# Optimization experiments

Measured on AMD Instinct MI355X. Metric: run time of the kernel, lower is better.

Reference implementation:

```python
import jax, jax.numpy as jnp
import numpy as np

B, D = 90000, 100
E_GNN, E_MLP = 4, 4
E = E_GNN + E_MLP + 1  # 9
K = 2
NOISE_EPS = 0.01
LOSS_COEF = 0.4
GATE_MEAN, GATE_STD = 0.1, 1.0  # registered buffers in the torch module


def setup_inputs() -> dict:
    key = jax.random.key(0)
    ks = jax.random.split(key, 16)
    f = jax.random.normal
    return {
        "memory_feats": f(ks[0], (B, D), jnp.float32),
        "recent_raw": f(ks[1], (B, E_MLP, D), jnp.float32),
        "spatial_raw": f(ks[2], (B, E_GNN, D), jnp.float32),
        "node_feats_src": f(ks[3], (B, D), jnp.float32),
        "noise": f(ks[4], (B, E), jnp.float32),
        "deg_coef": f(ks[5], (1, D, 2), jnp.float32),
        "w_gate": f(ks[6], (6 * D, E), jnp.float32) * 0.05,
        "w_noise": f(ks[7], (6 * D, E), jnp.float32) * 0.05,
        "src_w": f(ks[8], (D, D), jnp.float32) * 0.1,
        "src_b": f(ks[9], (D,), jnp.float32) * 0.1,
        "dst_w": f(ks[10], (D, D), jnp.float32) * 0.1,
        "dst_b": f(ks[11], (D,), jnp.float32) * 0.1,
        "out_w": f(ks[12], (D, 1), jnp.float32) * 0.1,
        "out_b": f(ks[13], (1,), jnp.float32) * 0.1,
        "degree": jax.random.randint(ks[14], (B,), 0, 64, jnp.int32),
        "neg_samples": 1,
    }


def _cv_squared(x):
    # torch .var() is unbiased (ddof=1)
    return jnp.var(x, ddof=1) / (jnp.mean(x) ** 2 + 1e-10)


def _norm_cdf(v):
    return jax.scipy.stats.norm.cdf(v, loc=GATE_MEAN, scale=GATE_STD)


def reference(memory_feats, recent_raw, spatial_raw, node_feats_src, noise,
              deg_coef, w_gate, w_noise, src_w, src_b, dst_w, dst_b,
              out_w, out_b, degree, neg_samples):
    # memory expert output (dropout is identity in eval; relu applied)
    mem = jax.nn.relu(memory_feats)                        # [B, D]
    rec = jax.nn.relu(recent_raw)                          # [B, Em, D]
    log_deg = jnp.log(degree.astype(mem.dtype) + 1.0)      # [B]
    # degree-conditioned reweighting: stack([r, r*log_deg],-1) * deg_coef, sum(-1)
    c0, c1 = deg_coef[0, :, 0], deg_coef[0, :, 1]          # [D]
    spa = spatial_raw * (c0 + log_deg[:, None, None] * c1)  # [B, Eg, D]

    combine = jnp.concatenate([mem[:, None, :], spa, rec], axis=1)  # [B, E, D]
    result_spa = spa.mean(axis=1)
    result_rec = rec.mean(axis=1)
    x1 = mem + result_spa + result_rec
    x2 = mem * result_spa * result_rec
    cat = jnp.concatenate([mem, result_spa, result_rec, x1, x2, node_feats_src], axis=1)  # [B, 6D]

    # noisy top-k gating (train=True)
    clean = cat @ w_gate                                   # [B, E]
    std = jax.nn.softplus(cat @ w_noise) + NOISE_EPS
    noisy = clean + noise * std
    top_vals, top_idx = jax.lax.top_k(noisy, K + 1)        # [B, K+1]
    topk_gates = jax.nn.softmax(top_vals[:, :K], axis=1)
    b_idx = jnp.arange(noisy.shape[0])[:, None]
    gates = jnp.zeros_like(noisy).at[b_idx, top_idx[:, :K]].set(topk_gates)

    # prob of being in top-k for load-balance loss
    thr_in = top_vals[:, K][:, None]
    thr_out = top_vals[:, K - 1][:, None]
    is_in = noisy > thr_in
    prob = jnp.where(is_in,
                     _norm_cdf((clean - thr_in) / std),
                     _norm_cdf((clean - thr_out) / std))
    load = prob.sum(axis=0)
    importance = gates.sum(axis=0)
    loss = LOSS_COEF * (_cv_squared(importance) + _cv_squared(load))

    out = jnp.einsum('bed,be->bd', combine, gates)         # [B, D]

    # edge predictor
    num_edge = out.shape[0] // (neg_samples + 2)
    h_src = out[:num_edge] @ src_w + src_b
    h_pos = out[num_edge:2 * num_edge] @ dst_w + dst_b
    h_neg = out[2 * num_edge:] @ dst_w + dst_b
    pos = jax.nn.relu(h_src + h_pos) @ out_w + out_b       # [num_edge, 1]
    neg = jax.nn.relu(jnp.tile(h_src, (neg_samples, 1)) + h_neg) @ out_w + out_b
    return pos, neg, loss
```

## Files before the change

kernel.cpp:

```cpp
#include <hip/hip_runtime.h>
#include <math.h>

#define DD 100

#define DPP_ADD(v, ctrl) ((v) + __int_as_float(__builtin_amdgcn_update_dpp( \
    0, __float_as_int(v), (ctrl), 0xf, 0xf, true)))

__device__ __forceinline__ float blo(unsigned u){
  union { unsigned i; float f; } c; c.i = u << 16; return c.f;
}
__device__ __forceinline__ float bhi(unsigned u){
  union { unsigned i; float f; } c; c.i = u & 0xFFFF0000u; return c.f;
}
__device__ __forceinline__ unsigned short f2bf(float f){
  unsigned u = __float_as_uint(f);
  unsigned r = (u + 0x7FFFu + ((u >> 16) & 1u)) >> 16;
  return (unsigned short)r;
}
__device__ __forceinline__ float phi_fast(float z){
  float x  = z * 0.70710678118654752440f;
  float ax = fabsf(x);
  float t  = __builtin_amdgcn_rcpf(1.0f + 0.3275911f*ax);
  float p  = t*(0.254829592f + t*(-0.284496736f + t*(1.421413741f
           + t*(-1.453152027f + t*1.061405429f))));
  float e  = __expf(-ax*ax);
  float erfv = copysignf(1.0f - p*e, x);
  return 0.5f*(1.0f + erfv);
}
__device__ __forceinline__ float4 relu4(float4 v){
  return make_float4(fmaxf(v.x,0.f), fmaxf(v.y,0.f), fmaxf(v.z,0.f), fmaxf(v.w,0.f));
}

__global__ __launch_bounds__(256) void k_gate(
    const float* __restrict__ memf, const float* __restrict__ recr,
    const float* __restrict__ spar, const float* __restrict__ nsrc,
    const float* __restrict__ noise, const float* __restrict__ degc,
    const float* __restrict__ wg,   const float* __restrict__ wn,
    const int*   __restrict__ degree,
    float4* __restrict__ gateinfo, float* __restrict__ partials, int B)
{
  __shared__ __align__(16) float sWF[100*92];
  __shared__ __align__(16) float sC0[DD], sC1[DD];
  __shared__ float sPart[4][18];

  for (int i = threadIdx.x; i < 9000; i += 256){
    int d = i / 90, j2 = i % 90;
    int seg = j2 / 18, e = j2 % 18;
    int rowA = (seg==0) ? d : (seg==1) ? 100+d : (seg==2) ? 200+d
             : (seg==3) ? 400+d : 500+d;
    const float* W = (e < 9) ? wg : wn;
    int ee = (e < 9) ? e : e - 9;
    float v = W[rowA*9 + ee] + ((seg < 3) ? W[(300+d)*9 + ee] : 0.f);
    sWF[d*92 + j2] = v;
  }
  for (int i = threadIdx.x; i < DD; i += 256){ sC0[i]=degc[2*i]; sC1[i]=degc[2*i+1]; }
  __syncthreads();

  const int wave = threadIdx.x >> 6, lane = threadIdx.x & 63;
  const int fq = lane & 3, rl = lane >> 2;
  const float4* sC04 = (const float4*)sC0;
  const float4* sC14 = (const float4*)sC1;

  float ldA[9], imA[9];
  #pragma unroll
  for (int e = 0; e < 9; e++){ ldA[e]=0.f; imA[e]=0.f; }

  const int row = (blockIdx.x*4 + wave)*16 + rl;
  const bool valid = row < B;
  const int rc = valid ? row : B-1;
  {
    const float* pm = memf + (size_t)rc*DD;
    const float* ps = spar + (size_t)rc*4*DD;
    const float* pr = recr + (size_t)rc*4*DD;
    const float* pn = nsrc + (size_t)rc*DD;
    float ldg = __logf((float)degree[rc] + 1.0f);

    float cg[9], cn[9];
    #pragma unroll
    for (int e = 0; e < 9; e++){ cg[e]=0.f; cn[e]=0.f; }

    for (int k = 0; k < 7; k++){
      int c = fq + 4*k;
      float fz = (c < 25) ? 1.f : 0.f;
      int ce = (c < 25) ? c : 0;
      float4 me = *(const float4*)(pm + 4*ce);
      float4 s0 = *(const float4*)(ps + 0*DD + 4*ce);
      float4 s1 = *(const float4*)(ps + 1*DD + 4*ce);
      float4 s2 = *(const float4*)(ps + 2*DD + 4*ce);
      float4 s3 = *(const float4*)(ps + 3*DD + 4*ce);
      float4 r0 = *(const float4*)(pr + 0*DD + 4*ce);
      float4 r1 = *(const float4*)(pr + 1*DD + 4*ce);
      float4 r2 = *(const float4*)(pr + 2*DD + 4*ce);
      float4 r3 = *(const float4*)(pr + 3*DD + 4*ce);
      float4 nv = *(const float4*)(pn + 4*ce);
      float4 c04 = sC04[ce], c14 = sC14[ce];

      float4 m4 = relu4(me);
      float4 sc = make_float4(c04.x + ldg*c14.x, c04.y + ldg*c14.y,
                              c04.z + ldg*c14.z, c04.w + ldg*c14.w);
      float4 rs4 = make_float4((s0.x+s1.x+s2.x+s3.x)*0.25f*sc.x,
                               (s0.y+s1.y+s2.y+s3.y)*0.25f*sc.y,
                               (s0.z+s1.z+s2.z+s3.z)*0.25f*sc.z,
                               (s0.w+s1.w+s2.w+s3.w)*0.25f*sc.w);
      float4 a0 = relu4(r0), a1 = relu4(r1), a2 = relu4(r2), a3 = relu4(r3);
      float4 rr4 = make_float4((a0.x+a1.x+a2.x+a3.x)*0.25f,
                               (a0.y+a1.y+a2.y+a3.y)*0.25f,
                               (a0.z+a1.z+a2.z+a3.z)*0.25f,
                               (a0.w+a1.w+a2.w+a3.w)*0.25f);
      m4.x*=fz; m4.y*=fz; m4.z*=fz; m4.w*=fz;
      rs4.x*=fz; rs4.y*=fz; rs4.z*=fz; rs4.w*=fz;
      rr4.x*=fz; rr4.y*=fz; rr4.z*=fz; rr4.w*=fz;
      float4 ns4 = make_float4(nv.x*fz, nv.y*fz, nv.z*fz, nv.w*fz);
      float4 x24 = make_float4(m4.x*rs4.x*rr4.x, m4.y*rs4.y*rr4.y,
                               m4.z*rs4.z*rr4.z, m4.w*rs4.w*rr4.w);

      #pragma unroll
      for (int j = 0; j < 4; j++){
        const float der0 = (j==0)?m4.x :(j==1)?m4.y :(j==2)?m4.z :m4.w;
        const float der1 = (j==0)?rs4.x:(j==1)?rs4.y:(j==2)?rs4.z:rs4.w;
        const float der2 = (j==0)?rr4.x:(j==1)?rr4.y:(j==2)?rr4.z:rr4.w;
        const float der3 = (j==0)?x24.x:(j==1)?x24.y:(j==2)?x24.z:x24.w;
        const float der4 = (j==0)?ns4.x:(j==1)?ns4.y:(j==2)?ns4.z:ns4.w;
        const float4* wpj = (const float4*)(sWF + (4*ce + j)*92);
        #pragma unroll
        for (int t = 0; t < 23; t++){
          float4 w = wpj[t];
          #pragma unroll
          for (int u = 0; u < 4; u++){
            const int ww = 4*t + u;
            if (ww < 90){
              const int seg = ww/18, e = ww%18;
              float wv = (u==0)?w.x:(u==1)?w.y:(u==2)?w.z:w.w;
              float dv = (seg==0)?der0:(seg==1)?der1:(seg==2)?der2:(seg==3)?der3:der4;
              if (e < 9) cg[e] += dv*wv; else cn[e-9] += dv*wv;
            }
          }
        }
      }
    }

    #pragma unroll
    for (int e = 0; e < 9; e++){
      cg[e] = DPP_ADD(cg[e], 0xB1); cg[e] = DPP_ADD(cg[e], 0x4E);
      cn[e] = DPP_ADD(cn[e], 0xB1); cn[e] = DPP_ADD(cn[e], 0x4E);
    }

    float sd[9], rsd[9], nz[9];
    #pragma unroll
    for (int e = 0; e < 9; e++){
      float x = cn[e];
      float spl = fmaxf(x, 0.f) + __logf(1.0f + __expf(-fabsf(x)));
      sd[e]  = spl + 0.01f;
      rsd[e] = __builtin_amdgcn_rcpf(sd[e]);
      nz[e]  = cg[e] + noise[(size_t)rc*9 + e] * sd[e];
    }
    float v1 = -3.402823e38f, v2 = v1, v3 = v1; int i1 = -1, i2 = -1;
    #pragma unroll
    for (int e = 0; e < 9; e++){
      float v = nz[e];
      if (v > v1){ v3=v2; v2=v1; i2=i1; v1=v; i1=e; }
      else if (v > v2){ v3=v2; v2=v; i2=e; }
      else if (v > v3){ v3=v; }
    }
    float t  = __expf(v2 - v1);
    float g1 = __builtin_amdgcn_rcpf(1.0f + t);
    float g2 = t*g1;
    if (valid){
      #pragma unroll
      for (int e = 0; e < 9; e++){
        float thr = (nz[e] > v3) ? v3 : v2;
        float z = (cg[e] - thr)*rsd[e] - 0.1f;
        ldA[e] += phi_fast(z);
        imA[e] += (e==i1) ? g1 : ((e==i2) ? g2 : 0.f);
      }
      if (fq == 0)
        gateinfo[row] = make_float4(g1, g2, __int_as_float(i1), __int_as_float(i2));
    }
  }

  #pragma unroll
  for (int e = 0; e < 9; e++){
    #pragma unroll
    for (int off = 4; off < 64; off <<= 1){
      ldA[e] += __shfl_xor(ldA[e], off, 64);
      imA[e] += __shfl_xor(imA[e], off, 64);
    }
  }
  if (lane == 0){
    #pragma unroll
    for (int e = 0; e < 9; e++){ sPart[wave][e] = imA[e]; sPart[wave][9+e] = ldA[e]; }
  }
  __syncthreads();
  if (threadIdx.x < 18){
    float s = sPart[0][threadIdx.x] + sPart[1][threadIdx.x]
            + sPart[2][threadIdx.x] + sPart[3][threadIdx.x];
    partials[blockIdx.x*18 + threadIdx.x] = s;
  }
}

__global__ __launch_bounds__(256) void k_mix(
    const float* __restrict__ memf, const float* __restrict__ recr,
    const float* __restrict__ spar, const float* __restrict__ degc,
    const int* __restrict__ degree, const float4* __restrict__ gateinfo,
    float* __restrict__ outm, int B)
{
  const int total = B*25;
  for (int idx = blockIdx.x*256 + threadIdx.x; idx < total; idx += gridDim.x*256){
    int row = idx / 25, q = idx - row*25;
    float4 gi = gateinfo[row];
    float gv[2] = {gi.x, gi.y};
    int   ei[2] = {__float_as_int(gi.z), __float_as_int(gi.w)};
    float4 acc = make_float4(0.f,0.f,0.f,0.f);
    #pragma unroll
    for (int s = 0; s < 2; s++){
      int e = ei[s]; float g = gv[s];
      float4 v;
      if (e == 0){
        v = relu4(*(const float4*)(memf + (size_t)row*DD + 4*q));
      } else if (e < 5){
        float ldg = __logf((float)degree[row] + 1.0f);
        float4 ca = *(const float4*)(degc + 8*q);
        float4 cb = *(const float4*)(degc + 8*q + 4);
        float4 sv = *(const float4*)(spar + ((size_t)row*4 + (e-1))*DD + 4*q);
        v = make_float4(sv.x*(ca.x + ldg*ca.y), sv.y*(ca.z + ldg*ca.w),
                        sv.z*(cb.x + ldg*cb.y), sv.w*(cb.z + ldg*cb.w));
      } else {
        v = relu4(*(const float4*)(recr + ((size_t)row*4 + (e-5))*DD + 4*q));
      }
      acc.x += g*v.x; acc.y += g*v.y; acc.z += g*v.z; acc.w += g*v.w;
    }
    ((float4*)outm)[(size_t)row*25 + q] = acc;
  }
}

__global__ __launch_bounds__(1024) void k_loss(const float* __restrict__ partials,
                                               int nblk, float* __restrict__ dloss)
{
  __shared__ float sS[18][57];
  int t = threadIdx.x;
  if (t < 1008){
    int k = t % 18, c = t / 18;
    float s = 0.f;
    for (int b = c; b < nblk; b += 56) s += partials[b*18 + k];
    sS[k][c] = s;
  }
  __syncthreads();
  if (t < 18){
    float tot = 0.f;
    #pragma unroll
    for (int c = 0; c < 56; c++) tot += sS[t][c];
    sS[t][56] = tot;
  }
  __syncthreads();
  if (t == 0){
    float mi = 0.f, ml = 0.f;
    #pragma unroll
    for (int e = 0; e < 9; e++){ mi += sS[e][56]; ml += sS[9+e][56]; }
    mi *= (1.f/9.f); ml *= (1.f/9.f);
    float vi = 0.f, vl = 0.f;
    #pragma unroll
    for (int e = 0; e < 9; e++){
      float a = sS[e][56]   - mi; vi += a*a;
      float b = sS[9+e][56] - ml; vl += b*b;
    }
    vi *= (1.f/8.f); vl *= (1.f/8.f);
    *dloss = 0.4f * (vi/(mi*mi + 1e-10f) + vl/(ml*ml + 1e-10f));
  }
}

__global__ __launch_bounds__(512) void k_edge(
    const float* __restrict__ om,
    const float* __restrict__ sw, const float* __restrict__ sb,
    const float* __restrict__ dw, const float* __restrict__ db,
    const float* __restrict__ ow, const float* __restrict__ ob,
    float* __restrict__ dout, int NE)
{
  __shared__ __align__(4) unsigned short sSW[DD*102];
  __shared__ __align__(4) unsigned short sDW[DD*102];
  __shared__ float sSB[DD], sDB[DD], sOW[DD];

  for (int i = threadIdx.x; i < DD*DD; i += 512){
    int k = i / DD, d = i % DD;
    sSW[d*102 + k] = f2bf(sw[i]);
    sDW[d*102 + k] = f2bf(dw[i]);
  }
  for (int i = threadIdx.x; i < DD; i += 512){ sSB[i]=sb[i]; sDB[i]=db[i]; sOW[i]=ow[i]; }
  __syncthreads();

  const int wave = threadIdx.x >> 6, lane = threadIdx.x & 63;
  const int grp = blockIdx.x*8 + wave;
  const int e0 = grp*4;
  if (e0 >= NE) return;
  const int e0u = __builtin_amdgcn_readfirstlane(e0);
  const float* oS = om + (size_t)e0u*DD;
  const float* oP = om + ((size_t)(NE  + e0u))*DD;
  const float* oN = om + ((size_t)(2*NE + e0u))*DD;
  const int d0 = lane, d1 = lane + 64;
  const bool h1 = (d1 < DD);
  const int dc1 = h1 ? d1 : 0;

  float aS[4][2], aP[4][2], aN[4][2];
  #pragma unroll
  for (int r = 0; r < 4; r++){
    aS[r][0]=0.f; aS[r][1]=0.f; aP[r][0]=0.f; aP[r][1]=0.f; aN[r][0]=0.f; aN[r][1]=0.f;
  }

  for (int k = 0; k < DD; k += 4){
    unsigned uA = *(const unsigned*)&sSW[d0 *102 + k];
    unsigned uB = *(const unsigned*)&sSW[d0 *102 + k + 2];
    unsigned uC = *(const unsigned*)&sSW[dc1*102 + k];
    unsigned uD = *(const unsigned*)&sSW[dc1*102 + k + 2];
    unsigned uE = *(const unsigned*)&sDW[d0 *102 + k];
    unsigned uF = *(const unsigned*)&sDW[d0 *102 + k + 2];
    unsigned uG = *(const unsigned*)&sDW[dc1*102 + k];
    unsigned uH = *(const unsigned*)&sDW[dc1*102 + k + 2];
    float wS00=blo(uA), wS01=bhi(uA), wS02=blo(uB), wS03=bhi(uB);
    float wS10=blo(uC), wS11=bhi(uC), wS12=blo(uD), wS13=bhi(uD);
    float wD00=blo(uE), wD01=bhi(uE), wD02=blo(uF), wD03=bhi(uF);
    float wD10=blo(uG), wD11=bhi(uG), wD12=blo(uH), wD13=bhi(uH);
    #pragma unroll
    for (int r = 0; r < 4; r++){
      float4 ov = *(const float4*)(oS + r*DD + k);
      float4 pv = *(const float4*)(oP + r*DD + k);
      float4 nv = *(const float4*)(oN + r*DD + k);
      aS[r][0] += ov.x*wS00 + ov.y*wS01 + ov.z*wS02 + ov.w*wS03;
      aS[r][1] += ov.x*wS10 + ov.y*wS11 + ov.z*wS12 + ov.w*wS13;
      aP[r][0] += pv.x*wD00 + pv.y*wD01 + pv.z*wD02 + pv.w*wD03;
      aP[r][1] += pv.x*wD10 + pv.y*wD11 + pv.z*wD12 + pv.w*wD13;
      aN[r][0] += nv.x*wD00 + nv.y*wD01 + nv.z*wD02 + nv.w*wD03;
      aN[r][1] += nv.x*wD10 + nv.y*wD11 + nv.z*wD12 + nv.w*wD13;
    }
  }

  float owa = sOW[d0], owb = sOW[dc1];
  float sba = sSB[d0], sbb = sSB[dc1];
  float dba = sDB[d0], dbb = sDB[dc1];
  float ob0 = ob[0];
  #pragma unroll
  for (int r = 0; r < 4; r++){
    float hs0 = aS[r][0] + sba, hp0 = aP[r][0] + dba, hn0 = aN[r][0] + dba;
    float tp = fmaxf(hs0 + hp0, 0.f)*owa;
    float tn = fmaxf(hs0 + hn0, 0.f)*owa;
    if (h1){
      float hs1 = aS[r][1] + sbb, hp1 = aP[r][1] + dbb, hn1 = aN[r][1] + dbb;
      tp += fmaxf(hs1 + hp1, 0.f)*owb;
      tn += fmaxf(hs1 + hn1, 0.f)*owb;
    }
    #pragma unroll
    for (int off = 32; off > 0; off >>= 1){
      tp += __shfl_xor(tp, off, 64);
      tn += __shfl_xor(tn, off, 64);
    }
    if (lane == 0){
      dout[e0 + r]      = tp + ob0;
      dout[NE + e0 + r] = tn + ob0;
    }
  }
}

extern "C" void kernel_launch(void* const* d_in, const int* in_sizes, int n_in,
                              void* d_out, int out_size, void* d_ws, size_t ws_size,
                              hipStream_t stream)
{
  (void)n_in; (void)out_size; (void)ws_size;
  const float* memf  = (const float*)d_in[0];
  const float* recr  = (const float*)d_in[1];
  const float* spar  = (const float*)d_in[2];
  const float* nsrc  = (const float*)d_in[3];
  const float* noise = (const float*)d_in[4];
  const float* degc  = (const float*)d_in[5];
  const float* wg    = (const float*)d_in[6];
  const float* wn    = (const float*)d_in[7];
  const float* sw    = (const float*)d_in[8];
  const float* sb    = (const float*)d_in[9];
  const float* dw    = (const float*)d_in[10];
  const float* db    = (const float*)d_in[11];
  const float* ow    = (const float*)d_in[12];
  const float* ob    = (const float*)d_in[13];
  const int*   deg   = (const int*)d_in[14];

  const int B  = in_sizes[0] / DD;
  const int NE = B / 3;
  const int blocksA = (B + 63) / 64;

  float4* gateinfo = (float4*)d_ws;
  float*  outm     = (float*)(gateinfo + B);
  float*  partials = outm + (size_t)B*DD;
  float*  dout     = (float*)d_out;

  k_gate<<<dim3(blocksA), dim3(256), 0, stream>>>(memf, recr, spar, nsrc, noise,
                                                  degc, wg, wn, deg, gateinfo,
                                                  partials, B);
  k_mix<<<dim3(2048), dim3(256), 0, stream>>>(memf, recr, spar, degc, deg,
                                              gateinfo, outm, B);
  k_loss<<<dim3(1), dim3(1024), 0, stream>>>(partials, blocksA, dout + 2*NE);
  const int blocks2 = (NE/4 + 7) / 8;
  k_edge<<<dim3(blocks2), dim3(512), 0, stream>>>(outm, sw, sb, dw, db, ow, ob, dout, NE);
}
```

Measured before the change: 286.1 us.

## Move gate weight folding to separate kernel and give each row its own thread

The folded gate/noise weight matrix is now built once by a small k_fold kernel into workspace, replacing the per-block rebuild into shared memory. k_gate shrinks to 64-thread blocks with one thread per row. Each thread walks all 25 float4 chunks with double-buffered register loads, and reads the weights through uniform global/scalar loads, which removes the DPP cross-lane reduction and the block sync. The trade-offs are a per-thread stride of 1600 bytes across rows, which gives uncoalesced input loads, higher register pressure, and an extra kernel launch.

```diff
diff --git a/kernel.cpp b/kernel.cpp
--- a/kernel.cpp
+++ b/kernel.cpp
@@ -2,9 +2,6 @@
 #include <math.h>
 
 #define DD 100
-
-#define DPP_ADD(v, ctrl) ((v) + __int_as_float(__builtin_amdgcn_update_dpp( \
-    0, __float_as_int(v), (ctrl), 0xf, 0xf, true)))
 
 __device__ __forceinline__ float blo(unsigned u){
   union { unsigned i; float f; } c; c.i = u << 16; return c.f;
@@ -31,170 +28,139 @@
   return make_float4(fmaxf(v.x,0.f), fmaxf(v.y,0.f), fmaxf(v.z,0.f), fmaxf(v.w,0.f));
 }
 
-__global__ __launch_bounds__(256) void k_gate(
+__global__ void k_fold(const float* __restrict__ wg, const float* __restrict__ wn,
+                       float* __restrict__ wfold)
+{
+  int idx = blockIdx.x*256 + threadIdx.x;
+  if (idx >= 9000) return;
+  int dim = idx/90, r = idx%90, s = r/18, e = r%18;
+  const float* W = (e < 9) ? wg : wn;
+  int ee = (e < 9) ? e : e-9;
+  int rowA = (s==0) ? dim : (s==1) ? 100+dim : (s==2) ? 200+dim
+           : (s==3) ? 400+dim : 500+dim;
+  float v = W[rowA*9 + ee] + ((s < 3) ? W[(300+dim)*9 + ee] : 0.f);
+  wfold[idx] = v;
+}
+
+struct Quad { float4 me, s0, s1, s2, s3, r0, r1, r2, r3, nv; };
+
+__device__ __forceinline__ void loadq(Quad& Q, const float* pm, const float* ps,
+                                      const float* pr, const float* pn, int q){
+  Q.me = *(const float4*)(pm + 4*q);
+  Q.s0 = *(const float4*)(ps + 0*DD + 4*q);
+  Q.s1 = *(const float4*)(ps + 1*DD + 4*q);
+  Q.s2 = *(const float4*)(ps + 2*DD + 4*q);
+  Q.s3 = *(const float4*)(ps + 3*DD + 4*q);
+  Q.r0 = *(const float4*)(pr + 0*DD + 4*q);
+  Q.r1 = *(const float4*)(pr + 1*DD + 4*q);
+  Q.r2 = *(const float4*)(pr + 2*DD + 4*q);
+  Q.r3 = *(const float4*)(pr + 3*DD + 4*q);
+  Q.nv = *(const float4*)(pn + 4*q);
+}
+
+#define GETJ(v) ((j==0)?(v).x:(j==1)?(v).y:(j==2)?(v).z:(v).w)
+
+__device__ __forceinline__ void bodyq(const Quad& Q, const float* __restrict__ wfold,
+                                      const float* __restrict__ degc, float ldg,
+                                      float* cg, float* cn, int q){
+  #pragma unroll
+  for (int j = 0; j < 4; j++){
+    const int dim = 4*q + j;
+    float c0 = degc[2*dim], c1 = degc[2*dim+1];
+    float mm = fmaxf(GETJ(Q.me), 0.f);
+    float sc = c0 + ldg*c1;
+    float rs = (GETJ(Q.s0)+GETJ(Q.s1)+GETJ(Q.s2)+GETJ(Q.s3))*0.25f*sc;
+    float rr = (fmaxf(GETJ(Q.r0),0.f)+fmaxf(GETJ(Q.r1),0.f)
+               +fmaxf(GETJ(Q.r2),0.f)+fmaxf(GETJ(Q.r3),0.f))*0.25f;
+    float x2 = mm*rs*rr;
+    float ns = GETJ(Q.nv);
+    const float* w = wfold + (size_t)dim*90;
+    #pragma unroll
+    for (int e = 0; e < 9; e++){
+      cg[e] += mm*w[e]    + rs*w[18+e] + rr*w[36+e] + x2*w[54+e] + ns*w[72+e];
+      cn[e] += mm*w[9+e]  + rs*w[27+e] + rr*w[45+e] + x2*w[63+e] + ns*w[81+e];
+    }
+  }
+}
+
+__global__ __launch_bounds__(64) void k_gate(
     const float* __restrict__ memf, const float* __restrict__ recr,
     const float* __restrict__ spar, const float* __restrict__ nsrc,
     const float* __restrict__ noise, const float* __restrict__ degc,
-    const float* __restrict__ wg,   const float* __restrict__ wn,
-    const int*   __restrict__ degree,
+    const float* __restrict__ wfold, const int* __restrict__ degree,
     float4* __restrict__ gateinfo, float* __restrict__ partials, int B)
 {
-  __shared__ __align__(16) float sWF[100*92];
-  __shared__ __align__(16) float sC0[DD], sC1[DD];
-  __shared__ float sPart[4][18];
-
-  for (int i = threadIdx.x; i < 9000; i += 256){
-    int d = i / 90, j2 = i % 90;
-    int seg = j2 / 18, e = j2 % 18;
-    int rowA = (seg==0) ? d : (seg==1) ? 100+d : (seg==2) ? 200+d
-             : (seg==3) ? 400+d : 500+d;
-    const float* W = (e < 9) ? wg : wn;
-    int ee = (e < 9) ? e : e - 9;
-    float v = W[rowA*9 + ee] + ((seg < 3) ? W[(300+d)*9 + ee] : 0.f);
-    sWF[d*92 + j2] = v;
-  }
-  for (int i = threadIdx.x; i < DD; i += 256){ sC0[i]=degc[2*i]; sC1[i]=degc[2*i+1]; }
-  __syncthreads();
-
-  const int wave = threadIdx.x >> 6, lane = threadIdx.x & 63;
-  const int fq = lane & 3, rl = lane >> 2;
-  const float4* sC04 = (const float4*)sC0;
-  const float4* sC14 = (const float4*)sC1;
-
-  float ldA[9], imA[9];
-  #pragma unroll
-  for (int e = 0; e < 9; e++){ ldA[e]=0.f; imA[e]=0.f; }
-
-  const int row = (blockIdx.x*4 + wave)*16 + rl;
+  const int lane = threadIdx.x;
+  const int row  = blockIdx.x*64 + lane;
   const bool valid = row < B;
   const int rc = valid ? row : B-1;
-  {
-    const float* pm = memf + (size_t)rc*DD;
-    const float* ps = spar + (size_t)rc*4*DD;
-    const float* pr = recr + (size_t)rc*4*DD;
-    const float* pn = nsrc + (size_t)rc*DD;
-    float ldg = __logf((float)degree[rc] + 1.0f);
-
-    float cg[9], cn[9];
-    #pragma unroll
-    for (int e = 0; e < 9; e++){ cg[e]=0.f; cn[e]=0.f; }
-
-    for (int k = 0; k < 7; k++){
-      int c = fq + 4*k;
-      float fz = (c < 25) ? 1.f : 0.f;
-      int ce = (c < 25) ? c : 0;
-      float4 me = *(const float4*)(pm + 4*ce);
-      float4 s0 = *(const float4*)(ps + 0*DD + 4*ce);
-      float4 s1 = *(const float4*)(ps + 1*DD + 4*ce);
-      float4 s2 = *(const float4*)(ps + 2*DD + 4*ce);
-      float4 s3 = *(const float4*)(ps + 3*DD + 4*ce);
-      float4 r0 = *(const float4*)(pr + 0*DD + 4*ce);
-      float4 r1 = *(const float4*)(pr + 1*DD + 4*ce);
-      float4 r2 = *(const float4*)(pr + 2*DD + 4*ce);
-      float4 r3 = *(const float4*)(pr + 3*DD + 4*ce);
-      float4 nv = *(const float4*)(pn + 4*ce);
-      float4 c04 = sC04[ce], c14 = sC14[ce];
-
-      float4 m4 = relu4(me);
-      float4 sc = make_float4(c04.x + ldg*c14.x, c04.y + ldg*c14.y,
-                              c04.z + ldg*c14.z, c04.w + ldg*c14.w);
-      float4 rs4 = make_float4((s0.x+s1.x+s2.x+s3.x)*0.25f*sc.x,
-                               (s0.y+s1.y+s2.y+s3.y)*0.25f*sc.y,
-                               (s0.z+s1.z+s2.z+s3.z)*0.25f*sc.z,
-                               (s0.w+s1.w+s2.w+s3.w)*0.25f*sc.w);
-      float4 a0 = relu4(r0), a1 = relu4(r1), a2 = relu4(r2), a3 = relu4(r3);
-      float4 rr4 = make_float4((a0.x+a1.x+a2.x+a3.x)*0.25f,
-                               (a0.y+a1.y+a2.y+a3.y)*0.25f,
-                               (a0.z+a1.z+a2.z+a3.z)*0.25f,
-                               (a0.w+a1.w+a2.w+a3.w)*0.25f);
-      m4.x*=fz; m4.y*=fz; m4.z*=fz; m4.w*=fz;
-      rs4.x*=fz; rs4.y*=fz; rs4.z*=fz; rs4.w*=fz;
-      rr4.x*=fz; rr4.y*=fz; rr4.z*=fz; rr4.w*=fz;
-      float4 ns4 = make_float4(nv.x*fz, nv.y*fz, nv.z*fz, nv.w*fz);
-      float4 x24 = make_float4(m4.x*rs4.x*rr4.x, m4.y*rs4.y*rr4.y,
-                               m4.z*rs4.z*rr4.z, m4.w*rs4.w*rr4.w);
-
-      #pragma unroll
-      for (int j = 0; j < 4; j++){
-        const float der0 = (j==0)?m4.x :(j==1)?m4.y :(j==2)?m4.z :m4.w;
-        const float der1 = (j==0)?rs4.x:(j==1)?rs4.y:(j==2)?rs4.z:rs4.w;
-        const float der2 = (j==0)?rr4.x:(j==1)?rr4.y:(j==2)?rr4.z:rr4.w;
-        const float der3 = (j==0)?x24.x:(j==1)?x24.y:(j==2)?x24.z:x24.w;
-        const float der4 = (j==0)?ns4.x:(j==1)?ns4.y:(j==2)?ns4.z:ns4.w;
-        const float4* wpj = (const float4*)(sWF + (4*ce + j)*92);
-        #pragma unroll
-        for (int t = 0; t < 23; t++){
-          float4 w = wpj[t];
-          #pragma unroll
-          for (int u = 0; u < 4; u++){
-            const int ww = 4*t + u;
-            if (ww < 90){
-              const int seg = ww/18, e = ww%18;
-              float wv = (u==0)?w.x:(u==1)?w.y:(u==2)?w.z:w.w;
-              float dv = (seg==0)?der0:(seg==1)?der1:(seg==2)?der2:(seg==3)?der3:der4;
-              if (e < 9) cg[e] += dv*wv; else cn[e-9] += dv*wv;
-            }
-          }
-        }
-      }
-    }
-
+
+  const float* pm = memf + (size_t)rc*DD;
+  const float* ps = spar + (size_t)rc*4*DD;
+  const float* pr = recr + (size_t)rc*4*DD;
+  const float* pn = nsrc + (size_t)rc*DD;
+  float ldg = __logf((float)degree[rc] + 1.0f);
+
+  float cg[9], cn[9];
+  #pragma unroll
+  for (int e = 0; e < 9; e++){ cg[e]=0.f; cn[e]=0.f; }
+
+  Quad A, Bq;
+  loadq(A, pm, ps, pr, pn, 0);
+  for (int q = 0; q < 24; q += 2){
+    loadq(Bq, pm, ps, pr, pn, q+1);
+    bodyq(A, wfold, degc, ldg, cg, cn, q);
+    loadq(A, pm, ps, pr, pn, q+2);
+    bodyq(Bq, wfold, degc, ldg, cg, cn, q+1);
+  }
+  bodyq(A, wfold, degc, ldg, cg, cn, 24);
+
+  float sdv[9], rsd[9], nz[9];
+  #pragma unroll
+  for (int e = 0; e < 9; e++){
+    float x = cn[e];
+    float spl = fmaxf(x, 0.f) + __logf(1.0f + __expf(-fabsf(x)));
+    sdv[e] = spl + 0.01f;
+    rsd[e] = __builtin_amdgcn_rcpf(sdv[e]);
+    nz[e]  = cg[e] + noise[(size_t)rc*9 + e] * sdv[e];
+  }
+  float v1 = -3.402823e38f, v2 = v1, v3 = v1; int i1 = -1, i2 = -1;
+  #pragma unroll
+  for (int e = 0; e < 9; e++){
+    float v = nz[e];
+    if (v > v1){ v3=v2; v2=v1; i2=i1; v1=v; i1=e; }
+    else if (v > v2){ v3=v2; v2=v; i2=e; }
+    else if (v > v3){ v3=v; }
+  }
+  float t  = __expf(v2 - v1);
+  float g1 = __builtin_amdgcn_rcpf(1.0f + t);
+  float g2 = t*g1;
+
+  float ld[9], im[9];
+  #pragma unroll
+  for (int e = 0; e < 9; e++){
+    float thr = (nz[e] > v3) ? v3 : v2;
+    float z = (cg[e] - thr)*rsd[e] - 0.1f;
+    ld[e] = valid ? phi_fast(z) : 0.f;
+    im[e] = valid ? ((e==i1) ? g1 : ((e==i2) ? g2 : 0.f)) : 0.f;
+  }
+  if (valid)
+    gateinfo[row] = make_float4(g1, g2, __int_as_float(i1), __int_as_float(i2));
+
+  #pragma unroll
+  for (int e = 0; e < 9; e++){
+    #pragma unroll
+    for (int off = 1; off < 64; off <<= 1){
+      ld[e] += __shfl_xor(ld[e], off, 64);
+      im[e] += __shfl_xor(im[e], off, 64);
+    }
+  }
+  if (lane == 0){
     #pragma unroll
     for (int e = 0; e < 9; e++){
-      cg[e] = DPP_ADD(cg[e], 0xB1); cg[e] = DPP_ADD(cg[e], 0x4E);
-      cn[e] = DPP_ADD(cn[e], 0xB1); cn[e] = DPP_ADD(cn[e], 0x4E);
-    }
-
-    float sd[9], rsd[9], nz[9];
-    #pragma unroll
-    for (int e = 0; e < 9; e++){
-      float x = cn[e];
-      float spl = fmaxf(x, 0.f) + __logf(1.0f + __expf(-fabsf(x)));
-      sd[e]  = spl + 0.01f;
-      rsd[e] = __builtin_amdgcn_rcpf(sd[e]);
-      nz[e]  = cg[e] + noise[(size_t)rc*9 + e] * sd[e];
-    }
-    float v1 = -3.402823e38f, v2 = v1, v3 = v1; int i1 = -1, i2 = -1;
-    #pragma unroll
-    for (int e = 0; e < 9; e++){
-      float v = nz[e];
-      if (v > v1){ v3=v2; v2=v1; i2=i1; v1=v; i1=e; }
-      else if (v > v2){ v3=v2; v2=v; i2=e; }
-      else if (v > v3){ v3=v; }
-    }
-    float t  = __expf(v2 - v1);
-    float g1 = __builtin_amdgcn_rcpf(1.0f + t);
-    float g2 = t*g1;
-    if (valid){
-      #pragma unroll
-      for (int e = 0; e < 9; e++){
-        float thr = (nz[e] > v3) ? v3 : v2;
-        float z = (cg[e] - thr)*rsd[e] - 0.1f;
-        ldA[e] += phi_fast(z);
-        imA[e] += (e==i1) ? g1 : ((e==i2) ? g2 : 0.f);
-      }
-      if (fq == 0)
-        gateinfo[row] = make_float4(g1, g2, __int_as_float(i1), __int_as_float(i2));
-    }
-  }
-
-  #pragma unroll
-  for (int e = 0; e < 9; e++){
-    #pragma unroll
-    for (int off = 4; off < 64; off <<= 1){
-      ldA[e] += __shfl_xor(ldA[e], off, 64);
-      imA[e] += __shfl_xor(imA[e], off, 64);
-    }
-  }
-  if (lane == 0){
-    #pragma unroll
-    for (int e = 0; e < 9; e++){ sPart[wave][e] = imA[e]; sPart[wave][9+e] = ldA[e]; }
-  }
-  __syncthreads();
-  if (threadIdx.x < 18){
-    float s = sPart[0][threadIdx.x] + sPart[1][threadIdx.x]
-            + sPart[2][threadIdx.x] + sPart[3][threadIdx.x];
-    partials[blockIdx.x*18 + threadIdx.x] = s;
+      partials[blockIdx.x*18 + e]     = im[e];
+      partials[blockIdx.x*18 + 9 + e] = ld[e];
+    }
   }
 }
 
@@ -386,11 +352,13 @@
   float4* gateinfo = (float4*)d_ws;
   float*  outm     = (float*)(gateinfo + B);
   float*  partials = outm + (size_t)B*DD;
+  float*  wfold    = partials + (size_t)blocksA*18;
   float*  dout     = (float*)d_out;
 
-  k_gate<<<dim3(blocksA), dim3(256), 0, stream>>>(memf, recr, spar, nsrc, noise,
-                                                  degc, wg, wn, deg, gateinfo,
-                                                  partials, B);
+  k_fold<<<dim3(36), dim3(256), 0, stream>>>(wg, wn, wfold);
+  k_gate<<<dim3(blocksA), dim3(64), 0, stream>>>(memf, recr, spar, nsrc, noise,
+                                                 degc, wfold, deg, gateinfo,
+                                                 partials, B);
   k_mix<<<dim3(2048), dim3(256), 0, stream>>>(memf, recr, spar, degc, deg,
                                               gateinfo, outm, B);
   k_loss<<<dim3(1), dim3(1024), 0, stream>>>(partials, blocksA, dout + 2*NE);
```

Result: slower. 517.3 us (+80.8%).

## Precompute folded gate weights once and make gate kernel persistent grid-stride

Applied to the files above, without the earlier changes.

Moves the per-block folding of gate/noise weights into a separate small kernel that writes a 9000-float folded table to workspace. The gate kernel then runs a fixed 1024-block grid that loops over 64-row tiles, so each block fills its shared weight table once and reuses it across several tiles instead of rebuilding it for each of about 1400 blocks. The cost is an extra kernel launch, and partials now hold 1024 block entries. Fewer blocks may also lower occupancy or tail balance.

```diff
diff --git a/kernel.cpp b/kernel.cpp
--- a/kernel.cpp
+++ b/kernel.cpp
@@ -2,6 +2,7 @@
 #include <math.h>
 
 #define DD 100
+#define GGATE 1024
 
 #define DPP_ADD(v, ctrl) ((v) + __int_as_float(__builtin_amdgcn_update_dpp( \
     0, __float_as_int(v), (ctrl), 0xf, 0xf, true)))
@@ -31,28 +32,33 @@
   return make_float4(fmaxf(v.x,0.f), fmaxf(v.y,0.f), fmaxf(v.z,0.f), fmaxf(v.w,0.f));
 }
 
+__global__ void k_fold(const float* __restrict__ wg, const float* __restrict__ wn,
+                       float* __restrict__ wfold)
+{
+  int idx = blockIdx.x*256 + threadIdx.x;
+  if (idx >= 9000) return;
+  int dim = idx/90, r = idx%90, s = r/18, e = r%18;
+  const float* W = (e < 9) ? wg : wn;
+  int ee = (e < 9) ? e : e-9;
+  int rowA = (s==0) ? dim : (s==1) ? 100+dim : (s==2) ? 200+dim
+           : (s==3) ? 400+dim : 500+dim;
+  float v = W[rowA*9 + ee] + ((s < 3) ? W[(300+dim)*9 + ee] : 0.f);
+  wfold[idx] = v;
+}
+
 __global__ __launch_bounds__(256) void k_gate(
     const float* __restrict__ memf, const float* __restrict__ recr,
     const float* __restrict__ spar, const float* __restrict__ nsrc,
     const float* __restrict__ noise, const float* __restrict__ degc,
-    const float* __restrict__ wg,   const float* __restrict__ wn,
-    const int*   __restrict__ degree,
+    const float* __restrict__ wfold, const int* __restrict__ degree,
     float4* __restrict__ gateinfo, float* __restrict__ partials, int B)
 {
   __shared__ __align__(16) float sWF[100*92];
   __shared__ __align__(16) float sC0[DD], sC1[DD];
   __shared__ float sPart[4][18];
 
-  for (int i = threadIdx.x; i < 9000; i += 256){
-    int d = i / 90, j2 = i % 90;
-    int seg = j2 / 18, e = j2 % 18;
-    int rowA = (seg==0) ? d : (seg==1) ? 100+d : (seg==2) ? 200+d
-             : (seg==3) ? 400+d : 500+d;
-    const float* W = (e < 9) ? wg : wn;
-    int ee = (e < 9) ? e : e - 9;
-    float v = W[rowA*9 + ee] + ((seg < 3) ? W[(300+d)*9 + ee] : 0.f);
-    sWF[d*92 + j2] = v;
-  }
+  for (int i = threadIdx.x; i < 9000; i += 256)
+    sWF[(i/90)*92 + (i%90)] = wfold[i];
   for (int i = threadIdx.x; i < DD; i += 256){ sC0[i]=degc[2*i]; sC1[i]=degc[2*i+1]; }
   __syncthreads();
 
@@ -65,10 +71,11 @@
   #pragma unroll
   for (int e = 0; e < 9; e++){ ldA[e]=0.f; imA[e]=0.f; }
 
-  const int row = (blockIdx.x*4 + wave)*16 + rl;
-  const bool valid = row < B;
-  const int rc = valid ? row : B-1;
-  {
+  const int ntile = (B + 63) / 64;
+  for (int t = blockIdx.x; t < ntile; t += GGATE){
+    const int row = t*64 + wave*16 + rl;
+    const bool valid = row < B;
+    const int rc = valid ? row : B-1;
     const float* pm = memf + (size_t)rc*DD;
     const float* ps = spar + (size_t)rc*4*DD;
     const float* pr = recr + (size_t)rc*4*DD;
@@ -123,11 +130,11 @@
         const float der4 = (j==0)?ns4.x:(j==1)?ns4.y:(j==2)?ns4.z:ns4.w;
         const float4* wpj = (const float4*)(sWF + (4*ce + j)*92);
         #pragma unroll
-        for (int t = 0; t < 23; t++){
-          float4 w = wpj[t];
+        for (int tq = 0; tq < 23; tq++){
+          float4 w = wpj[tq];
           #pragma unroll
           for (int u = 0; u < 4; u++){
-            const int ww = 4*t + u;
+            const int ww = 4*tq + u;
             if (ww < 90){
               const int seg = ww/18, e = ww%18;
               float wv = (u==0)?w.x:(u==1)?w.y:(u==2)?w.z:w.w;
@@ -162,9 +169,9 @@
       else if (v > v2){ v3=v2; v2=v; i2=e; }
       else if (v > v3){ v3=v; }
     }
-    float t  = __expf(v2 - v1);
-    float g1 = __builtin_amdgcn_rcpf(1.0f + t);
-    float g2 = t*g1;
+    float tt = __expf(v2 - v1);
+    float g1 = __builtin_amdgcn_rcpf(1.0f + tt);
+    float g2 = tt*g1;
     if (valid){
       #pragma unroll
       for (int e = 0; e < 9; e++){
@@ -381,19 +388,20 @@
 
   const int B  = in_sizes[0] / DD;
   const int NE = B / 3;
-  const int blocksA = (B + 63) / 64;
 
   float4* gateinfo = (float4*)d_ws;
   float*  outm     = (float*)(gateinfo + B);
   float*  partials = outm + (size_t)B*DD;
+  float*  wfold    = partials + (size_t)GGATE*18;
   float*  dout     = (float*)d_out;
 
-  k_gate<<<dim3(blocksA), dim3(256), 0, stream>>>(memf, recr, spar, nsrc, noise,
-                                                  degc, wg, wn, deg, gateinfo,
-                                                  partials, B);
+  k_fold<<<dim3(36), dim3(256), 0, stream>>>(wg, wn, wfold);
+  k_gate<<<dim3(GGATE), dim3(256), 0, stream>>>(memf, recr, spar, nsrc, noise,
+                                                degc, wfold, deg, gateinfo,
+                                                partials, B);
   k_mix<<<dim3(2048), dim3(256), 0, stream>>>(memf, recr, spar, degc, deg,
                                               gateinfo, outm, B);
-  k_loss<<<dim3(1), dim3(1024), 0, stream>>>(partials, blocksA, dout + 2*NE);
+  k_loss<<<dim3(1), dim3(1024), 0, stream>>>(partials, GGATE, dout + 2*NE);
   const int blocks2 = (NE/4 + 7) / 8;
   k_edge<<<dim3(blocks2), dim3(512), 0, stream>>>(outm, sw, sb, dw, db, ow, ob, dout, NE);
 }
```

New measurement: 259.8 us. 1.1x faster.
